# Performance work log

Hardware: AMD Instinct MI355X
Metric: run time of the kernel (lower is better)

## Reference

```python
import jax, jax.numpy as jnp
import numpy as np
import math

B, L, DM, H, TD, K = 4, 1024, 1024, 16, 8, 8
D = DM // H  # head_dim = 64


def setup_inputs() -> dict:
    key = jax.random.key(0)
    ks = jax.random.split(key, 20)
    shape = (H, D, TD, K)
    inp = {
        'P': jax.random.normal(ks[0], (B, L, DM), jnp.float32),
        't': jax.random.uniform(ks[1], (B, L, TD), jnp.float32),
    }
    i = 2
    for nm in ('Q', 'K', 'V'):
        inp['mu_' + nm] = jax.random.normal(ks[i], shape, jnp.float32); i += 1
        inp['sigma_' + nm] = jnp.clip(jnp.abs(jax.random.normal(ks[i], shape, jnp.float32)), 0.001); i += 1
        inp['w_' + nm] = jax.random.normal(ks[i], shape, jnp.float32); i += 1
        inp['gamma_' + nm] = jnp.zeros((H, D), jnp.float32)
        inp['W_' + nm] = jax.random.normal(ks[i], (H, D, D), jnp.float32); i += 1
    inp['W_O_w'] = jax.random.normal(ks[i], (DM, DM), jnp.float32) * (1.0 / math.sqrt(DM)); i += 1
    inp['W_O_b'] = jnp.zeros((DM,), jnp.float32)
    return inp


def _gaussian_kernel(t, mu, sigma, w):
    # t: [B,L,T]; mu/sigma/w: [H,D,T,K] -> out [B,L,H,D]
    tt = t[:, :, None, None, :, None]              # [B,L,1,1,T,1]
    g = w * jnp.exp(-(tt - mu) ** 2 / (2.0 * sigma ** 2))  # [B,L,H,D,T,K]
    return g.sum(axis=(-1, -2))


def reference(P, t, mu_Q, sigma_Q, w_Q, gamma_Q, W_Q,
              mu_K, sigma_K, w_K, gamma_K, W_K,
              mu_V, sigma_V, w_V, gamma_V, W_V,
              W_O_w, W_O_b):
    Bv, Lv, _ = P.shape
    Ph = P.reshape(Bv, Lv, H, D)                    # [B,L,H,D]
    Q = _gaussian_kernel(t, mu_Q, sigma_Q, w_Q) * Ph + gamma_Q
    Kx = _gaussian_kernel(t, mu_K, sigma_K, w_K) * Ph + gamma_K
    V = _gaussian_kernel(t, mu_V, sigma_V, w_V) * Ph + gamma_V
    Q = jnp.einsum('blhd,hdf->blhf', Q, W_Q)
    Kx = jnp.einsum('blhd,hdf->blhf', Kx, W_K)
    V = jnp.einsum('blhd,hdf->blhf', V, W_V)
    scores = jnp.einsum('blhf,bmhf->bhlm', Q, Kx) / math.sqrt(D)
    A = jax.nn.softmax(scores, axis=-1)
    out = jnp.einsum('bhlm,bmhf->blhf', A, V).reshape(Bv, Lv, DM)
    return out @ W_O_w.T + W_O_b
```

## Files before the change

kernel.cpp:

```cpp
#include <hip/hip_runtime.h>
#include <cstdint>

#define DEVI __device__ __forceinline__

constexpr int Bc = 4, Lc = 1024, DMc = 1024, Hc = 16, TDc = 8, Kc = 8, Dc = 64;
constexpr int NBL = Bc * Lc;
constexpr int PAR = Hc * Dc * TDc * Kc;

using f16x8 = __attribute__((ext_vector_type(8))) _Float16;
using f16x4 = __attribute__((ext_vector_type(4))) _Float16;
using s16x8 = __attribute__((ext_vector_type(8))) short;
using s16x4 = __attribute__((ext_vector_type(4))) short;
using f32x4 = __attribute__((ext_vector_type(4))) float;
using f32x2 = __attribute__((ext_vector_type(2))) float;

DEVI unsigned short f2bf(float x){
  union { float f; unsigned u; } v; v.f = x;
  return (unsigned short)((v.u + 0x7fffu + ((v.u >> 16) & 1u)) >> 16);
}

DEVI unsigned cvtpk_bf16(float lo, float hi){
  unsigned r;
  asm("v_cvt_pk_bf16_f32 %0, %1, %2" : "=v"(r) : "v"(lo), "v"(hi));
  return r;
}

#define SWZ_ON 1
DEVI int swz(int row, int unit){
#if SWZ_ON
  return unit ^ (row & 7);
#else
  (void)row; return unit;
#endif
}

__global__ __launch_bounds__(256) void k0_alpha(
    const float* __restrict__ sQ, const float* __restrict__ sK, const float* __restrict__ sV,
    float* __restrict__ aQ, float* __restrict__ aK, float* __restrict__ aV)
{
  int i = blockIdx.x * 256 + threadIdx.x;
  if (i < PAR){
    const float c = 0.8493218002880191f;
    aQ[i] = c / sQ[i];
    aK[i] = c / sK[i];
    aV[i] = c / sV[i];
  }
}

__global__ __launch_bounds__(256) void k0_wo(const float* __restrict__ WO, unsigned short* __restrict__ WOb)
{
  int i = blockIdx.x * 256 + threadIdx.x;
  if (i < DMc * DMc) WOb[i] = f2bf(WO[i]);
}

__global__ __launch_bounds__(256) void k0_wsplit(
    const float* __restrict__ WQ, const float* __restrict__ WK, const float* __restrict__ WV,
    _Float16* __restrict__ Whi, _Float16* __restrict__ Wlo)
{
  int i = blockIdx.x * 256 + threadIdx.x;
  if (i >= 3 * Hc * 64 * 64) return;
  const int d = i & 63, f = (i >> 6) & 63, h = (i >> 12) & 15, p = i >> 16;
  const float* W = (p == 0) ? WQ : (p == 1) ? WK : WV;
  float v = W[((size_t)h * 64 + d) * 64 + f];
  if (p == 0) v *= 0.18033688011112042f;
  const _Float16 hi = (_Float16)v;
  Whi[i] = hi;
  Wlo[i] = (_Float16)(v - (float)hi);
}

__global__ __launch_bounds__(256) void k1_gauss(
    const float* __restrict__ P, const float* __restrict__ t,
    const float* __restrict__ mu0, const float* __restrict__ al0, const float* __restrict__ w0, const float* __restrict__ gm0,
    const float* __restrict__ mu1, const float* __restrict__ al1, const float* __restrict__ w1, const float* __restrict__ gm1,
    const float* __restrict__ mu2, const float* __restrict__ al2, const float* __restrict__ w2, const float* __restrict__ gm2,
    float* __restrict__ o0, float* __restrict__ o1, float* __restrict__ o2)
{
  __shared__ float gbuf[64 * 65];
  const int h = blockIdx.x, tile = blockIdx.y, p = blockIdx.z;
  const int tid = threadIdx.x, lane = tid & 63;
  const int wv = __builtin_amdgcn_readfirstlane(tid >> 6);
  const int bl0 = tile * 64;

  const float* mu = (p == 0) ? mu0 : (p == 1) ? mu1 : mu2;
  const float* al = (p == 0) ? al0 : (p == 1) ? al1 : al2;
  const float* wp = (p == 0) ? w0  : (p == 1) ? w1  : w2;
  const float* gm = (p == 0) ? gm0 : (p == 1) ? gm1 : gm2;
  float*       op = (p == 0) ? o0  : (p == 1) ? o1  : o2;

  float tv[8];
  {
    const float4 t0 = *(const float4*)&t[(size_t)(bl0 + lane) * 8];
    const float4 t1 = *(const float4*)&t[(size_t)(bl0 + lane) * 8 + 4];
    tv[0] = t0.x; tv[1] = t0.y; tv[2] = t0.z; tv[3] = t0.w;
    tv[4] = t1.x; tv[5] = t1.y; tv[6] = t1.z; tv[7] = t1.w;
  }

  #pragma unroll 2
  for (int dd = 0; dd < 16; ++dd){
    const int d = wv * 16 + dd;
    const int base = (h * 64 + d) * 64;
    f32x2 g01 = {0.f, 0.f}, g23 = {0.f, 0.f};
    #pragma unroll
    for (int td = 0; td < 8; ++td){
      const float tval = tv[td];
      const f32x2 tt2 = {tval, tval};
      #pragma unroll
      for (int kk = 0; kk < 4; ++kk){
        const int idx = base + td * 8 + kk * 2;
        const f32x2 m2 = *(const f32x2*)&mu[idx];
        const f32x2 a2 = *(const f32x2*)&al[idx];
        const f32x2 w2 = *(const f32x2*)&wp[idx];
        const f32x2 u  = (tt2 - m2) * a2;
        const f32x2 nu = u * u;
        f32x2 e;
        e[0] = __builtin_amdgcn_exp2f(-nu[0]);
        e[1] = __builtin_amdgcn_exp2f(-nu[1]);
        if (kk & 1) g23 += w2 * e;
        else        g01 += w2 * e;
      }
    }
    gbuf[d * 65 + lane] = (g01[0] + g01[1]) + (g23[0] + g23[1]);
  }
  __syncthreads();

  {
    const int dl = tid & 63, rq = tid >> 6;
    const float gam = gm[h * 64 + dl];
    #pragma unroll 4
    for (int rr = 0; rr < 16; ++rr){
      const int r = rq * 16 + rr;
      const float g  = gbuf[dl * 65 + r];
      const float ph = P[(size_t)(bl0 + r) * DMc + h * 64 + dl];
      op[(size_t)(bl0 + r) * DMc + h * 64 + dl] = fmaf(g, ph, gam);
    }
  }
}

__global__ __launch_bounds__(256) void k2m(
    const float* __restrict__ Qg, const float* __restrict__ Kg, const float* __restrict__ Vg,
    const _Float16* __restrict__ Wsp_hi, const _Float16* __restrict__ Wsp_lo,
    _Float16* __restrict__ Qhi, _Float16* __restrict__ Qlo,
    _Float16* __restrict__ Khi, _Float16* __restrict__ Klo,
    unsigned short* __restrict__ Vt)
{
  __shared__ __align__(16) _Float16 XhiL[64 * 64];
  __shared__ __align__(16) _Float16 XloL[64 * 64];
  __shared__ __align__(16) _Float16 WhiL[64 * 64];
  __shared__ __align__(16) _Float16 WloL[64 * 64];
  const int h = blockIdx.x, tile = blockIdx.y, p = blockIdx.z;
  const int tid = threadIdx.x, lane = tid & 63, wv = tid >> 6;
  const int lrow = lane & 15, lgrp = lane >> 4;
  const int bl0 = tile * 64;

  const float* Xg = (p == 0) ? Qg : (p == 1) ? Kg : Vg;

  for (int i = tid; i < 1024; i += 256){
    const int row = i >> 4, c4 = i & 15;
    const float4 x = *(const float4*)&Xg[(size_t)(bl0 + row) * DMc + h * 64 + c4 * 4];
    const float xs[4] = {x.x, x.y, x.z, x.w};
    f16x4 hx, lx;
    #pragma unroll
    for (int j = 0; j < 4; ++j){
      hx[j] = (_Float16)xs[j];
      lx[j] = (_Float16)(xs[j] - (float)hx[j]);
    }
    const int off = row * 128 + swz(row, c4 >> 1) * 16 + (c4 & 1) * 8;
    *(f16x4*)((char*)XhiL + off) = hx;
    *(f16x4*)((char*)XloL + off) = lx;
  }
  {
    const _Float16* wh = Wsp_hi + ((size_t)p * Hc + h) * 4096;
    const _Float16* wl = Wsp_lo + ((size_t)p * Hc + h) * 4096;
    for (int i = tid; i < 512; i += 256){
      const int f = i >> 3, u = i & 7;
      *(f16x8*)((char*)WhiL + f * 128 + swz(f, u) * 16) = *(const f16x8*)(wh + f * 64 + u * 8);
      *(f16x8*)((char*)WloL + f * 128 + swz(f, u) * 16) = *(const f16x8*)(wl + f * 64 + u * 8);
    }
  }
  __syncthreads();

  f32x4 acc[4] = {};
  if (p < 2){
    #pragma unroll
    for (int ks = 0; ks < 2; ++ks){
      const int arow = wv * 16 + lrow;
      const int aoff = arow * 128 + swz(arow, ks * 4 + lgrp) * 16;
      f16x8 xh = *(const f16x8*)((const char*)XhiL + aoff);
      f16x8 xl = *(const f16x8*)((const char*)XloL + aoff);
      #pragma unroll
      for (int tf = 0; tf < 4; ++tf){
        const int brow = tf * 16 + lrow;
        const int boff = brow * 128 + swz(brow, ks * 4 + lgrp) * 16;
        f16x8 wh_ = *(const f16x8*)((const char*)WhiL + boff);
        f16x8 wl_ = *(const f16x8*)((const char*)WloL + boff);
        acc[tf] = __builtin_amdgcn_mfma_f32_16x16x32_f16(xh, wh_, acc[tf], 0, 0, 0);
        acc[tf] = __builtin_amdgcn_mfma_f32_16x16x32_f16(xl, wh_, acc[tf], 0, 0, 0);
        acc[tf] = __builtin_amdgcn_mfma_f32_16x16x32_f16(xh, wl_, acc[tf], 0, 0, 0);
      }
    }
  } else {
    #pragma unroll
    for (int ks = 0; ks < 2; ++ks){
      const int arow = wv * 16 + lrow;
      const int aoff = arow * 128 + swz(arow, ks * 4 + lgrp) * 16;
      f16x8 wh_ = *(const f16x8*)((const char*)WhiL + aoff);
      f16x8 wl_ = *(const f16x8*)((const char*)WloL + aoff);
      #pragma unroll
      for (int mt = 0; mt < 4; ++mt){
        const int brow = mt * 16 + lrow;
        const int boff = brow * 128 + swz(brow, ks * 4 + lgrp) * 16;
        f16x8 xh = *(const f16x8*)((const char*)XhiL + boff);
        f16x8 xl = *(const f16x8*)((const char*)XloL + boff);
        acc[mt] = __builtin_amdgcn_mfma_f32_16x16x32_f16(wh_, xh, acc[mt], 0, 0, 0);
        acc[mt] = __builtin_amdgcn_mfma_f32_16x16x32_f16(wl_, xh, acc[mt], 0, 0, 0);
        acc[mt] = __builtin_amdgcn_mfma_f32_16x16x32_f16(wh_, xl, acc[mt], 0, 0, 0);
      }
    }
  }

  const int b = bl0 >> 10, l0 = bl0 & 1023;
  if (p == 0){
    #pragma unroll
    for (int tf = 0; tf < 4; ++tf){
      const int f = tf * 16 + lrow;
      #pragma unroll
      for (int r = 0; r < 4; ++r){
        const int l = l0 + wv * 16 + lgrp * 4 + r;
        const float a = acc[tf][r];
        const _Float16 hi = (_Float16)a;
        const _Float16 lo = (_Float16)(a - (float)hi);
        const size_t o = (((size_t)b * Hc + h) * Lc + l) * 64 + f;
        Qhi[o] = hi; Qlo[o] = lo;
      }
    }
  } else if (p == 1){
    #pragma unroll
    for (int tf = 0; tf < 4; ++tf){
      const int f = tf * 16 + lrow;
      #pragma unroll
      for (int r = 0; r < 4; ++r){
        const int l = l0 + wv * 16 + lgrp * 4 + r;
        const float a = acc[tf][r];
        const _Float16 hi = (_Float16)a;
        const _Float16 lo = (_Float16)(a - (float)hi);
        const size_t o = (((size_t)b * Hc + h) * Lc + l) * 64 + (swz(l, f >> 3) << 3) + (f & 7);
        Khi[o] = hi; Klo[o] = lo;
      }
    }
  } else {
    const size_t basev = (((size_t)b * Hc + h) * 64) * Lc + l0;
    #pragma unroll
    for (int mt = 0; mt < 4; ++mt){
      const int ml = mt * 16 + lrow;
      #pragma unroll
      for (int r = 0; r < 4; ++r){
        const int f = wv * 16 + lgrp * 4 + r;
        Vt[basev + (size_t)f * Lc + (swz(f, ml >> 3) << 3) + (ml & 7)] = f2bf(acc[mt][r]);
      }
    }
  }
}

__global__ __launch_bounds__(256) void k3_attn(
    const _Float16* __restrict__ Qhi, const _Float16* __restrict__ Qlo,
    const _Float16* __restrict__ Khi, const _Float16* __restrict__ Klo,
    const unsigned short* __restrict__ Vt,
    unsigned short* __restrict__ AO)
{
  __shared__ __align__(16) _Float16 KhiL[64 * 64];
  __shared__ __align__(16) _Float16 KloL[64 * 64];
  __shared__ __align__(16) unsigned short VL[64 * 64];
  __shared__ __align__(16) unsigned short PL[4][16 * 64];
  const int bh = blockIdx.x, qt = blockIdx.y;
  const int tid = threadIdx.x, wv = tid >> 6, lane = tid & 63;
  const int lrow = lane & 15, lgrp = lane >> 4;
  const size_t bhL = (size_t)bh * Lc;

  f16x8 qh[2], ql[2];
  {
    const int qrow = qt * 64 + wv * 16 + lrow;
    const _Float16* q1 = &Qhi[(bhL + qrow) * 64 + lgrp * 8];
    const _Float16* q2 = &Qlo[(bhL + qrow) * 64 + lgrp * 8];
    qh[0] = *(const f16x8*)q1; qh[1] = *(const f16x8*)(q1 + 32);
    ql[0] = *(const f16x8*)q2; ql[1] = *(const f16x8*)(q2 + 32);
  }

  f32x4 o[4] = {};
  float mrun = -1e30f, lrun = 0.f;

  const int i0 = tid, i1 = tid + 256;
  const char* kbase = (const char*)(Khi + bhL * 64);
  const char* lbase = (const char*)(Klo + bhL * 64);
  const char* vbase = (const char*)(Vt + (size_t)bh * 64 * Lc);
  const int voff0 = (i0 >> 3) * 2048 + (i0 & 7) * 16;
  const int voff1 = (i1 >> 3) * 2048 + (i1 & 7) * 16;

  f16x8 ra0 = *(const f16x8*)(kbase + i0 * 16);
  f16x8 ra1 = *(const f16x8*)(kbase + i1 * 16);
  f16x8 rb0 = *(const f16x8*)(lbase + i0 * 16);
  f16x8 rb1 = *(const f16x8*)(lbase + i1 * 16);
  s16x8 rc0 = *(const s16x8*)(vbase + voff0);
  s16x8 rc1 = *(const s16x8*)(vbase + voff1);

  #pragma unroll 1
  for (int kt = 0; kt < 16; ++kt){
    __syncthreads();
    *(f16x8*)((char*)KhiL + i0 * 16) = ra0;
    *(f16x8*)((char*)KhiL + i1 * 16) = ra1;
    *(f16x8*)((char*)KloL + i0 * 16) = rb0;
    *(f16x8*)((char*)KloL + i1 * 16) = rb1;
    *(s16x8*)((char*)VL + i0 * 16) = rc0;
    *(s16x8*)((char*)VL + i1 * 16) = rc1;
    if (kt + 1 < 16){
      const char* kn = kbase + (kt + 1) * 8192;
      const char* ln = lbase + (kt + 1) * 8192;
      const char* vn = vbase + (kt + 1) * 128;
      ra0 = *(const f16x8*)(kn + i0 * 16);
      ra1 = *(const f16x8*)(kn + i1 * 16);
      rb0 = *(const f16x8*)(ln + i0 * 16);
      rb1 = *(const f16x8*)(ln + i1 * 16);
      rc0 = *(const s16x8*)(vn + voff0);
      rc1 = *(const s16x8*)(vn + voff1);
    }
    __syncthreads();

    f32x4 s[4] = {};
    #pragma unroll
    for (int tt = 0; tt < 4; ++tt){
      #pragma unroll
      for (int ks = 0; ks < 2; ++ks){
        const int m = tt * 16 + lrow;
        const int off = m * 128 + swz(m, ks * 4 + lgrp) * 16;
        f16x8 kh_ = *(const f16x8*)((const char*)KhiL + off);
        f16x8 kl_ = *(const f16x8*)((const char*)KloL + off);
        s[tt] = __builtin_amdgcn_mfma_f32_16x16x32_f16(kh_, qh[ks], s[tt], 0, 0, 0);
        s[tt] = __builtin_amdgcn_mfma_f32_16x16x32_f16(kh_, ql[ks], s[tt], 0, 0, 0);
        s[tt] = __builtin_amdgcn_mfma_f32_16x16x32_f16(kl_, qh[ks], s[tt], 0, 0, 0);
      }
    }

    float v;
    {
      float v0 = fmaxf(fmaxf(s[0][0], s[0][1]), fmaxf(s[0][2], s[0][3]));
      float v1 = fmaxf(fmaxf(s[1][0], s[1][1]), fmaxf(s[1][2], s[1][3]));
      float v2 = fmaxf(fmaxf(s[2][0], s[2][1]), fmaxf(s[2][2], s[2][3]));
      float v3 = fmaxf(fmaxf(s[3][0], s[3][1]), fmaxf(s[3][2], s[3][3]));
      v = fmaxf(fmaxf(v0, v1), fmaxf(v2, v3));
      v = fmaxf(v, __shfl_xor(v, 16));
      v = fmaxf(v, __shfl_xor(v, 32));
    }
    const float mn = fmaxf(mrun, v);
    const float sc = __builtin_amdgcn_exp2f(mrun - mn);
    mrun = mn;

    float rs = 0.f;
    float pp[4][4];
    #pragma unroll
    for (int tt = 0; tt < 4; ++tt){
      #pragma unroll
      for (int r = 0; r < 4; ++r){
        const float p = __builtin_amdgcn_exp2f(s[tt][r] - mn);
        rs += p;
        pp[tt][r] = p;
      }
    }
    rs += __shfl_xor(rs, 16);
    rs += __shfl_xor(rs, 32);
    lrun = lrun * sc + rs;
    #pragma unroll
    for (int t2 = 0; t2 < 4; ++t2){
      o[t2][0] *= sc; o[t2][1] *= sc; o[t2][2] *= sc; o[t2][3] *= sc;
    }

    short* pw = (short*)PL[wv];
    #pragma unroll
    for (int tt = 0; tt < 4; ++tt){
      uint2 pk;
      pk.x = cvtpk_bf16(pp[tt][0], pp[tt][1]);
      pk.y = cvtpk_bf16(pp[tt][2], pp[tt][3]);
      const int off = lrow * 128 + swz(lrow, tt * 2 + (lgrp >> 1)) * 16 + (lgrp & 1) * 8;
      *(uint2*)((char*)pw + off) = pk;
    }
    asm volatile("s_waitcnt lgkmcnt(0)" ::: "memory");
    __builtin_amdgcn_sched_barrier(0);

    #pragma unroll
    for (int ks = 0; ks < 2; ++ks){
      const int poff = lrow * 128 + swz(lrow, ks * 4 + lgrp) * 16;
      s16x8 pa = *(const s16x8*)((const char*)pw + poff);
      #pragma unroll
      for (int t2 = 0; t2 < 4; ++t2){
        const int f = t2 * 16 + lrow;
        const int voff = f * 128 + swz(f, ks * 4 + lgrp) * 16;
        s16x8 vb = *(const s16x8*)((const char*)VL + voff);
        o[t2] = __builtin_amdgcn_mfma_f32_16x16x32_bf16(vb, pa, o[t2], 0, 0, 0);
      }
    }
  }

  const int b = bh >> 4, hh = bh & 15;
  const float inv = 1.0f / lrun;
  const int l = qt * 64 + wv * 16 + lrow;
  unsigned short* aorow = &AO[((size_t)(b * Lc + l)) * DMc + hh * 64];
  #pragma unroll
  for (int t2 = 0; t2 < 4; ++t2){
    uint2 ov;
    ov.x = cvtpk_bf16(o[t2][0] * inv, o[t2][1] * inv);
    ov.y = cvtpk_bf16(o[t2][2] * inv, o[t2][3] * inv);
    *(uint2*)(aorow + t2 * 16 + lgrp * 4) = ov;
  }
}

__global__ __launch_bounds__(256) void k4_out(
    const unsigned short* __restrict__ A, const unsigned short* __restrict__ Bw,
    const float* __restrict__ bias, float* __restrict__ out)
{
  __shared__ __align__(16) unsigned short Asl[128 * 64];
  __shared__ __align__(16) unsigned short Bsl[128 * 64];
  const int mt = blockIdx.x, nt = blockIdx.y;
  const int tid = threadIdx.x, wv = tid >> 6, lane = tid & 63;
  const int wr = wv >> 1, wc = wv & 1, lrow = lane & 15, lgrp = lane >> 4;
  f32x4 acc[4][4] = {};
  const char* abase = (const char*)A  + (size_t)mt * 128 * 2048;
  const char* bbase = (const char*)Bw + (size_t)nt * 128 * 2048;

  for (int kt = 0; kt < 16; ++kt){
    __syncthreads();
    #pragma unroll
    for (int q = 0; q < 4; ++q){
      const int i = q * 256 + tid, row = i >> 3, u = i & 7;
      s16x8 av = *(const s16x8*)(abase + (size_t)row * 2048 + kt * 128 + u * 16);
      s16x8 bv = *(const s16x8*)(bbase + (size_t)row * 2048 + kt * 128 + u * 16);
      *(s16x8*)((char*)Asl + row * 128 + swz(row, u) * 16) = av;
      *(s16x8*)((char*)Bsl + row * 128 + swz(row, u) * 16) = bv;
    }
    __syncthreads();
    #pragma unroll
    for (int ks = 0; ks < 2; ++ks){
      s16x8 af[4], bf[4];
      #pragma unroll
      for (int i4 = 0; i4 < 4; ++i4){
        const int row = wr * 64 + i4 * 16 + lrow;
        af[i4] = *(const s16x8*)((const char*)Asl + row * 128 + swz(row, ks * 4 + lgrp) * 16);
        const int col = wc * 64 + i4 * 16 + lrow;
        bf[i4] = *(const s16x8*)((const char*)Bsl + col * 128 + swz(col, ks * 4 + lgrp) * 16);
      }
      #pragma unroll
      for (int i4 = 0; i4 < 4; ++i4)
        #pragma unroll
        for (int j4 = 0; j4 < 4; ++j4)
          acc[i4][j4] = __builtin_amdgcn_mfma_f32_16x16x32_bf16(af[i4], bf[j4], acc[i4][j4], 0, 0, 0);
    }
  }
  #pragma unroll
  for (int i4 = 0; i4 < 4; ++i4)
    #pragma unroll
    for (int j4 = 0; j4 < 4; ++j4){
      const int col = nt * 128 + wc * 64 + j4 * 16 + lrow;
      const float bb = bias[col];
      #pragma unroll
      for (int r = 0; r < 4; ++r){
        const int row = mt * 128 + wr * 64 + i4 * 16 + lgrp * 4 + r;
        out[(size_t)row * DMc + col] = acc[i4][j4][r] + bb;
      }
    }
}

extern "C" void kernel_launch(void* const* d_in, const int* in_sizes, int n_in,
                              void* d_out, int out_size, void* d_ws, size_t ws_size,
                              hipStream_t stream)
{
  const float* P   = (const float*)d_in[0];
  const float* t   = (const float*)d_in[1];
  const float* muQ = (const float*)d_in[2];
  const float* sgQ = (const float*)d_in[3];
  const float* wQ  = (const float*)d_in[4];
  const float* gQ  = (const float*)d_in[5];
  const float* WQ  = (const float*)d_in[6];
  const float* muK = (const float*)d_in[7];
  const float* sgK = (const float*)d_in[8];
  const float* wK  = (const float*)d_in[9];
  const float* gK  = (const float*)d_in[10];
  const float* WK  = (const float*)d_in[11];
  const float* muV = (const float*)d_in[12];
  const float* sgV = (const float*)d_in[13];
  const float* wV  = (const float*)d_in[14];
  const float* gV  = (const float*)d_in[15];
  const float* WV  = (const float*)d_in[16];
  const float* WO  = (const float*)d_in[17];
  const float* WOb = (const float*)d_in[18];

  char* w = (char*)d_ws;
  auto take = [&](size_t bytes) -> char* {
    char* p = w; w += (bytes + 255) & ~(size_t)255; return p;
  };
  float* aQ = (float*)take((size_t)PAR * 4);
  float* aK = (float*)take((size_t)PAR * 4);
  float* aV = (float*)take((size_t)PAR * 4);
  float* Qg = (float*)take((size_t)NBL * DMc * 4);
  float* Kg = (float*)take((size_t)NBL * DMc * 4);
  float* Vg = (float*)take((size_t)NBL * DMc * 4);
  _Float16* Qhi = (_Float16*)take((size_t)NBL * DMc * 2);
  _Float16* Qlo = (_Float16*)take((size_t)NBL * DMc * 2);
  _Float16* Khi = (_Float16*)take((size_t)NBL * DMc * 2);
  _Float16* Klo = (_Float16*)take((size_t)NBL * DMc * 2);
  unsigned short* Vt    = (unsigned short*)take((size_t)NBL * DMc * 2);
  unsigned short* AO    = (unsigned short*)take((size_t)NBL * DMc * 2);
  unsigned short* WOb16 = (unsigned short*)take((size_t)DMc * DMc * 2);
  _Float16* Wsp_hi = (_Float16*)take((size_t)3 * Hc * 64 * 64 * 2);
  _Float16* Wsp_lo = (_Float16*)take((size_t)3 * Hc * 64 * 64 * 2);
  if ((size_t)(w - (char*)d_ws) > ws_size) return;

  k0_alpha<<<PAR / 256, 256, 0, stream>>>(sgQ, sgK, sgV, aQ, aK, aV);
  k0_wo<<<DMc * DMc / 256, 256, 0, stream>>>(WO, WOb16);
  k0_wsplit<<<(3 * Hc * 64 * 64) / 256, 256, 0, stream>>>(WQ, WK, WV, Wsp_hi, Wsp_lo);
  k1_gauss<<<dim3(Hc, NBL / 64, 3), 256, 0, stream>>>(P, t,
      muQ, aQ, wQ, gQ,  muK, aK, wK, gK,  muV, aV, wV, gV,  Qg, Kg, Vg);
  k2m<<<dim3(Hc, NBL / 64, 3), 256, 0, stream>>>(Qg, Kg, Vg, Wsp_hi, Wsp_lo,
      Qhi, Qlo, Khi, Klo, Vt);
  k3_attn<<<dim3(Bc * Hc, Lc / 64), 256, 0, stream>>>(Qhi, Qlo, Khi, Klo, Vt, AO);
  k4_out<<<dim3(NBL / 128, DMc / 128), 256, 0, stream>>>(AO, WOb16, WOb, (float*)d_out);
}
```

Before: 205.8 us.

## Fuse gaussian modulation kernel with per-head projection to drop fp32 intermediates

Merges the gaussian kernel and the per-head W projection into a single kernel. The modulated activations are kept in registers, split into fp16 hi/lo, and written into shared memory that reuses the gbuf region, so the three 16MB fp32 intermediate buffers are never written to or read from global memory. This removes one launch and roughly 96MB of HBM traffic. The cost is an extra barrier and higher register pressure in the combined kernel.

```diff
diff --git a/kernel.cpp b/kernel.cpp
--- a/kernel.cpp
+++ b/kernel.cpp
@@ -68,24 +68,43 @@
   Wlo[i] = (_Float16)(v - (float)hi);
 }
 
-__global__ __launch_bounds__(256) void k1_gauss(
+__global__ __launch_bounds__(256) void k12(
     const float* __restrict__ P, const float* __restrict__ t,
     const float* __restrict__ mu0, const float* __restrict__ al0, const float* __restrict__ w0, const float* __restrict__ gm0,
     const float* __restrict__ mu1, const float* __restrict__ al1, const float* __restrict__ w1, const float* __restrict__ gm1,
     const float* __restrict__ mu2, const float* __restrict__ al2, const float* __restrict__ w2, const float* __restrict__ gm2,
-    float* __restrict__ o0, float* __restrict__ o1, float* __restrict__ o2)
-{
-  __shared__ float gbuf[64 * 65];
+    const _Float16* __restrict__ Wsp_hi, const _Float16* __restrict__ Wsp_lo,
+    _Float16* __restrict__ Qhi, _Float16* __restrict__ Qlo,
+    _Float16* __restrict__ Khi, _Float16* __restrict__ Klo,
+    unsigned short* __restrict__ Vt)
+{
+  __shared__ __align__(16) char XU[64 * 65 * 4];
+  __shared__ __align__(16) _Float16 WhiL[64 * 64];
+  __shared__ __align__(16) _Float16 WloL[64 * 64];
+  float* gbuf = (float*)XU;
+  char* Xhi = XU;
+  char* Xlo = XU + 8192;
   const int h = blockIdx.x, tile = blockIdx.y, p = blockIdx.z;
   const int tid = threadIdx.x, lane = tid & 63;
   const int wv = __builtin_amdgcn_readfirstlane(tid >> 6);
+  const int lrow = lane & 15, lgrp = lane >> 4;
   const int bl0 = tile * 64;
 
   const float* mu = (p == 0) ? mu0 : (p == 1) ? mu1 : mu2;
   const float* al = (p == 0) ? al0 : (p == 1) ? al1 : al2;
   const float* wp = (p == 0) ? w0  : (p == 1) ? w1  : w2;
   const float* gm = (p == 0) ? gm0 : (p == 1) ? gm1 : gm2;
-  float*       op = (p == 0) ? o0  : (p == 1) ? o1  : o2;
+
+  {
+    const _Float16* wh = Wsp_hi + ((size_t)p * Hc + h) * 4096;
+    const _Float16* wl = Wsp_lo + ((size_t)p * Hc + h) * 4096;
+    #pragma unroll
+    for (int i = tid; i < 512; i += 256){
+      const int f = i >> 3, u = i & 7;
+      *(f16x8*)((char*)WhiL + f * 128 + swz(f, u) * 16) = *(const f16x8*)(wh + f * 64 + u * 8);
+      *(f16x8*)((char*)WloL + f * 128 + swz(f, u) * 16) = *(const f16x8*)(wl + f * 64 + u * 8);
+    }
+  }
 
   float tv[8];
   {
@@ -123,6 +142,7 @@
   }
   __syncthreads();
 
+  float xr[16];
   {
     const int dl = tid & 63, rq = tid >> 6;
     const float gam = gm[h * 64 + dl];
@@ -131,50 +151,24 @@
       const int r = rq * 16 + rr;
       const float g  = gbuf[dl * 65 + r];
       const float ph = P[(size_t)(bl0 + r) * DMc + h * 64 + dl];
-      op[(size_t)(bl0 + r) * DMc + h * 64 + dl] = fmaf(g, ph, gam);
-    }
-  }
-}
-
-__global__ __launch_bounds__(256) void k2m(
-    const float* __restrict__ Qg, const float* __restrict__ Kg, const float* __restrict__ Vg,
-    const _Float16* __restrict__ Wsp_hi, const _Float16* __restrict__ Wsp_lo,
-    _Float16* __restrict__ Qhi, _Float16* __restrict__ Qlo,
-    _Float16* __restrict__ Khi, _Float16* __restrict__ Klo,
-    unsigned short* __restrict__ Vt)
-{
-  __shared__ __align__(16) _Float16 XhiL[64 * 64];
-  __shared__ __align__(16) _Float16 XloL[64 * 64];
-  __shared__ __align__(16) _Float16 WhiL[64 * 64];
-  __shared__ __align__(16) _Float16 WloL[64 * 64];
-  const int h = blockIdx.x, tile = blockIdx.y, p = blockIdx.z;
-  const int tid = threadIdx.x, lane = tid & 63, wv = tid >> 6;
-  const int lrow = lane & 15, lgrp = lane >> 4;
-  const int bl0 = tile * 64;
-
-  const float* Xg = (p == 0) ? Qg : (p == 1) ? Kg : Vg;
-
-  for (int i = tid; i < 1024; i += 256){
-    const int row = i >> 4, c4 = i & 15;
-    const float4 x = *(const float4*)&Xg[(size_t)(bl0 + row) * DMc + h * 64 + c4 * 4];
-    const float xs[4] = {x.x, x.y, x.z, x.w};
-    f16x4 hx, lx;
-    #pragma unroll
-    for (int j = 0; j < 4; ++j){
-      hx[j] = (_Float16)xs[j];
-      lx[j] = (_Float16)(xs[j] - (float)hx[j]);
-    }
-    const int off = row * 128 + swz(row, c4 >> 1) * 16 + (c4 & 1) * 8;
-    *(f16x4*)((char*)XhiL + off) = hx;
-    *(f16x4*)((char*)XloL + off) = lx;
-  }
+      xr[rr] = fmaf(g, ph, gam);
+    }
+  }
+  __syncthreads();
+
   {
-    const _Float16* wh = Wsp_hi + ((size_t)p * Hc + h) * 4096;
-    const _Float16* wl = Wsp_lo + ((size_t)p * Hc + h) * 4096;
-    for (int i = tid; i < 512; i += 256){
-      const int f = i >> 3, u = i & 7;
-      *(f16x8*)((char*)WhiL + f * 128 + swz(f, u) * 16) = *(const f16x8*)(wh + f * 64 + u * 8);
-      *(f16x8*)((char*)WloL + f * 128 + swz(f, u) * 16) = *(const f16x8*)(wl + f * 64 + u * 8);
+    const int dl = tid & 63, rq = tid >> 6;
+    const int ub = swz(0, dl >> 3);
+    (void)ub;
+    #pragma unroll 4
+    for (int rr = 0; rr < 16; ++rr){
+      const int r = rq * 16 + rr;
+      const float a = xr[rr];
+      const _Float16 hi = (_Float16)a;
+      const _Float16 lo = (_Float16)(a - (float)hi);
+      const int off = r * 128 + swz(r, dl >> 3) * 16 + (dl & 7) * 2;
+      *(_Float16*)(Xhi + off) = hi;
+      *(_Float16*)(Xlo + off) = lo;
     }
   }
   __syncthreads();
@@ -185,8 +179,8 @@
     for (int ks = 0; ks < 2; ++ks){
       const int arow = wv * 16 + lrow;
       const int aoff = arow * 128 + swz(arow, ks * 4 + lgrp) * 16;
-      f16x8 xh = *(const f16x8*)((const char*)XhiL + aoff);
-      f16x8 xl = *(const f16x8*)((const char*)XloL + aoff);
+      f16x8 xh = *(const f16x8*)(Xhi + aoff);
+      f16x8 xl = *(const f16x8*)(Xlo + aoff);
       #pragma unroll
       for (int tf = 0; tf < 4; ++tf){
         const int brow = tf * 16 + lrow;
@@ -209,8 +203,8 @@
       for (int mt = 0; mt < 4; ++mt){
         const int brow = mt * 16 + lrow;
         const int boff = brow * 128 + swz(brow, ks * 4 + lgrp) * 16;
-        f16x8 xh = *(const f16x8*)((const char*)XhiL + boff);
-        f16x8 xl = *(const f16x8*)((const char*)XloL + boff);
+        f16x8 xh = *(const f16x8*)(Xhi + boff);
+        f16x8 xl = *(const f16x8*)(Xlo + boff);
         acc[mt] = __builtin_amdgcn_mfma_f32_16x16x32_f16(wh_, xh, acc[mt], 0, 0, 0);
         acc[mt] = __builtin_amdgcn_mfma_f32_16x16x32_f16(wl_, xh, acc[mt], 0, 0, 0);
         acc[mt] = __builtin_amdgcn_mfma_f32_16x16x32_f16(wh_, xl, acc[mt], 0, 0, 0);
@@ -497,9 +491,6 @@
   float* aQ = (float*)take((size_t)PAR * 4);
   float* aK = (float*)take((size_t)PAR * 4);
   float* aV = (float*)take((size_t)PAR * 4);
-  float* Qg = (float*)take((size_t)NBL * DMc * 4);
-  float* Kg = (float*)take((size_t)NBL * DMc * 4);
-  float* Vg = (float*)take((size_t)NBL * DMc * 4);
   _Float16* Qhi = (_Float16*)take((size_t)NBL * DMc * 2);
   _Float16* Qlo = (_Float16*)take((size_t)NBL * DMc * 2);
   _Float16* Khi = (_Float16*)take((size_t)NBL * DMc * 2);
@@ -514,10 +505,9 @@
   k0_alpha<<<PAR / 256, 256, 0, stream>>>(sgQ, sgK, sgV, aQ, aK, aV);
   k0_wo<<<DMc * DMc / 256, 256, 0, stream>>>(WO, WOb16);
   k0_wsplit<<<(3 * Hc * 64 * 64) / 256, 256, 0, stream>>>(WQ, WK, WV, Wsp_hi, Wsp_lo);
-  k1_gauss<<<dim3(Hc, NBL / 64, 3), 256, 0, stream>>>(P, t,
-      muQ, aQ, wQ, gQ,  muK, aK, wK, gK,  muV, aV, wV, gV,  Qg, Kg, Vg);
-  k2m<<<dim3(Hc, NBL / 64, 3), 256, 0, stream>>>(Qg, Kg, Vg, Wsp_hi, Wsp_lo,
-      Qhi, Qlo, Khi, Klo, Vt);
+  k12<<<dim3(Hc, NBL / 64, 3), 256, 0, stream>>>(P, t,
+      muQ, aQ, wQ, gQ,  muK, aK, wK, gK,  muV, aV, wV, gV,
+      Wsp_hi, Wsp_lo, Qhi, Qlo, Khi, Klo, Vt);
   k3_attn<<<dim3(Bc * Hc, Lc / 64), 256, 0, stream>>>(Qhi, Qlo, Khi, Klo, Vt, AO);
   k4_out<<<dim3(NBL / 128, DMc / 128), 256, 0, stream>>>(AO, WOb16, WOb, (float*)d_out);
 }
```

Result: slower. 214.6 us (+4.3%).
